# Optimization experiments

Hardware: AMD Instinct MI355X
Metric: run time of the kernel (lower is better)

The kernel has to match this reference:

```python
import jax, jax.numpy as jnp
import numpy as np

N_NODES = 100000
N_EDGES = 1600000
IN_DIM = 256
HID = 128
FUSE = 64


def setup_inputs() -> dict:
    key = jax.random.key(0)
    ks = jax.random.split(key, 10)
    x = jax.random.normal(ks[0], (N_NODES, IN_DIM), dtype=jnp.float32)
    edge_index = jax.random.randint(ks[1], (2, N_EDGES), 0, N_NODES, dtype=jnp.int64)
    h_node = jax.random.normal(ks[2], (N_NODES,), dtype=jnp.float32)
    s = 0.05
    W_homo = jax.random.normal(ks[3], (IN_DIM, HID), dtype=jnp.float32) * s
    b_homo = jnp.zeros((HID,), dtype=jnp.float32)
    W_het = jax.random.normal(ks[4], (IN_DIM, HID), dtype=jnp.float32) * s
    b_het = jnp.zeros((HID,), dtype=jnp.float32)
    W_fuse = jax.random.normal(ks[5], (HID, FUSE), dtype=jnp.float32) * s
    b_fuse = jnp.zeros((FUSE,), dtype=jnp.float32)
    W_cls = jax.random.normal(ks[6], (FUSE, 2), dtype=jnp.float32) * s
    b_cls = jnp.zeros((2,), dtype=jnp.float32)
    return {
        "x": x, "edge_index": edge_index, "h_node": h_node,
        "W_homo": W_homo, "b_homo": b_homo,
        "W_het": W_het, "b_het": b_het,
        "W_fuse": W_fuse, "b_fuse": b_fuse,
        "W_cls": W_cls, "b_cls": b_cls,
    }


def gcn_conv(x, edge_index, W, b):
    # PyG GCNConv: xw = x @ W, add self-loops, symmetric D^-1/2 (A+I) D^-1/2 aggregation, + bias
    n = x.shape[0]
    xw = x @ W  # [N, H] transform first (in_dim > hid keeps edge traffic small)
    loop = jnp.arange(n, dtype=edge_index.dtype)
    src = jnp.concatenate([edge_index[0], loop])
    dst = jnp.concatenate([edge_index[1], loop])
    deg = jax.ops.segment_sum(jnp.ones_like(dst, dtype=xw.dtype), dst, num_segments=n)
    dinv = jnp.where(deg > 0, jax.lax.rsqrt(deg), 0.0)
    norm = dinv[src] * dinv[dst]  # [E+N]
    msg = xw[src] * norm[:, None]  # gather + scale  [E+N, H]
    agg = jax.ops.segment_sum(msg, dst, num_segments=n)  # scatter-add
    return agg + b


def reference(x, edge_index, h_node,
              W_homo, b_homo, W_het, b_het,
              W_fuse, b_fuse, W_cls, b_cls):
    h_homo = jax.nn.relu(gcn_conv(x, edge_index, W_homo, b_homo))
    h_het = jax.nn.relu(gcn_conv(x, edge_index, W_het, b_het))
    h_fused = 0.5 * h_homo + 0.5 * h_het  # fixed alpha = 0.5 (no het gate)
    h = jax.nn.relu(h_fused @ W_fuse + b_fuse)
    logits = h @ W_cls + b_cls
    return logits
```

## Files before the change

kernel.cpp:

```cpp
#include <hip/hip_runtime.h>

#define IN_DIM 256
#define CHUNK 8192
#define NBUCKET 1024

typedef __attribute__((ext_vector_type(8))) short short8;
typedef __attribute__((ext_vector_type(4))) float f32x4;
typedef unsigned int uint;
typedef unsigned short ushort;

__device__ __forceinline__ ushort f2bf(float x) {
    uint u = __float_as_uint(x);
    u += 0x7FFFu + ((u >> 16) & 1u);
    return (ushort)(u >> 16);
}

__global__ __launch_bounds__(256) void hist_kernel(const int* __restrict__ dst,
                                                   int* __restrict__ hist_g,
                                                   int E, int NBLK) {
    __shared__ int h[NBUCKET];
    int tid = threadIdx.x;
#pragma unroll
    for (int i = 0; i < 4; ++i) h[tid + 256 * i] = 0;
    __syncthreads();
    int base = blockIdx.x * CHUNK;
#pragma unroll 4
    for (int i = 0; i < 32; ++i) {
        int e = base + i * 256 + tid;
        if (e < E) atomicAdd(&h[dst[e] >> 7], 1);
    }
    __syncthreads();
#pragma unroll
    for (int i = 0; i < 4; ++i) {
        int b = tid + 256 * i;
        hist_g[(size_t)b * NBLK + blockIdx.x] = h[b];
    }
}

__global__ __launch_bounds__(256) void block_sum_kernel(const int* __restrict__ d,
                                                        int* __restrict__ bsum, int L) {
    __shared__ int red[256];
    int base = blockIdx.x * 1024;
    int s = 0;
    for (int i = threadIdx.x; i < 1024; i += 256) {
        int idx = base + i;
        if (idx < L) s += d[idx];
    }
    red[threadIdx.x] = s;
    __syncthreads();
    for (int dd = 128; dd > 0; dd >>= 1) {
        if (threadIdx.x < dd) red[threadIdx.x] += red[threadIdx.x + dd];
        __syncthreads();
    }
    if (threadIdx.x == 0) bsum[blockIdx.x] = red[0];
}

__global__ __launch_bounds__(1024) void scan_sums_kernel(int* __restrict__ bsum, int B) {
    __shared__ int sh[1024];
    int t = threadIdx.x;
    sh[t] = (t < B) ? bsum[t] : 0;
    __syncthreads();
    for (int d = 1; d < 1024; d <<= 1) {
        int v = (t >= d) ? sh[t - d] : 0;
        __syncthreads();
        sh[t] += v;
        __syncthreads();
    }
    if (t < B) bsum[t] = (t == 0) ? 0 : sh[t - 1];
}

__global__ __launch_bounds__(256) void scan_apply_kernel(int* __restrict__ d,
                                                         const int* __restrict__ bsum, int L) {
    __shared__ int wsum[4];
    int lane = threadIdx.x & 63, wid = threadIdx.x >> 6;
    int idx = blockIdx.x * 1024 + threadIdx.x * 4;
    int c[4];
    int s = 0;
#pragma unroll
    for (int j = 0; j < 4; ++j) {
        c[j] = (idx + j < L) ? d[idx + j] : 0;
        s += c[j];
    }
    int incl = s;
#pragma unroll
    for (int dd = 1; dd < 64; dd <<= 1) {
        int v = __shfl_up(incl, dd);
        if (lane >= dd) incl += v;
    }
    if (lane == 63) wsum[wid] = incl;
    __syncthreads();
    int woff = 0;
    for (int i = 0; i < 4; ++i) woff += (i < wid) ? wsum[i] : 0;
    int excl = bsum[blockIdx.x] + woff + incl - s;
#pragma unroll
    for (int j = 0; j < 4; ++j) {
        if (idx + j < L) d[idx + j] = excl;
        excl += c[j];
    }
}

__global__ __launch_bounds__(256) void scatter_kernel(const int* __restrict__ ei,
                                                      const int* __restrict__ scanned,
                                                      uint2* __restrict__ sorted,
                                                      int E, int NBLK) {
    __shared__ int baseh[NBUCKET];
    __shared__ int curh[NBUCKET];
    int tid = threadIdx.x;
#pragma unroll
    for (int i = 0; i < 4; ++i) {
        int b = tid + 256 * i;
        baseh[b] = scanned[(size_t)b * NBLK + blockIdx.x];
        curh[b] = 0;
    }
    __syncthreads();
    int base = blockIdx.x * CHUNK;
#pragma unroll 4
    for (int i = 0; i < 32; ++i) {
        int e = base + i * 256 + tid;
        if (e < E) {
            int s = ei[e];
            int d = ei[E + e];
            int b = d >> 7;
            int r = atomicAdd(&curh[b], 1);
            sorted[baseh[b] + r] = make_uint2((uint)s, (uint)d);
        }
    }
}

__global__ __launch_bounds__(256) void bucket_csr_kernel(const uint2* __restrict__ sorted,
                                                         const int* __restrict__ scanned,
                                                         int* __restrict__ off,
                                                         int* __restrict__ csr,
                                                         float* __restrict__ dinv,
                                                         int N, int E, int NBLK) {
    __shared__ int cnt[128], cur[128];
    __shared__ int w0tot;
    int b = blockIdx.x;
    int tid = threadIdx.x;
    int estart = scanned[(size_t)b * NBLK];
    int eend = scanned[(size_t)(b + 1) * NBLK];
    if (tid < 128) cnt[tid] = 0;
    __syncthreads();
    for (int e = estart + tid; e < eend; e += 256)
        atomicAdd(&cnt[sorted[e].y & 127], 1);
    __syncthreads();
    int c = 0, incl = 0;
    if (tid < 128) {
        int lane = tid & 63;
        c = cnt[tid];
        incl = c;
#pragma unroll
        for (int d = 1; d < 64; d <<= 1) {
            int v = __shfl_up(incl, d);
            if (lane >= d) incl += v;
        }
        if (tid == 63) w0tot = incl;
    }
    __syncthreads();
    if (tid < 128) {
        int e0 = incl - c + ((tid >= 64) ? w0tot : 0);
        cur[tid] = e0;
        int node = b * 128 + tid;
        if (node < N) {
            off[node] = estart + e0;
            dinv[node] = rsqrtf((float)(c + 1));
        }
    }
    if (b == 0 && tid == 0) off[N] = E;
    __syncthreads();
    for (int e = estart + tid; e < eend; e += 256) {
        uint2 sd = sorted[e];
        int pos = atomicAdd(&cur[sd.y & 127], 1);
        csr[estart + pos] = (int)sd.x;
    }
}

__global__ void prep_kernel(const float* __restrict__ Wh, const float* __restrict__ Wt,
                            const float* __restrict__ Wf,
                            ushort* __restrict__ wT, ushort* __restrict__ WfB) {
    int b = blockIdx.x;
    int k = threadIdx.x;
    if (b < 256) {
        const float* W = (b < 128) ? Wh : Wt;
        wT[b * 256 + k] = f2bf(W[(size_t)k * 128 + (b & 127)]);
    } else {
        int col = b - 256;
        if (k < 128) WfB[col * 128 + k] = f2bf(Wf[(size_t)k * 64 + col]);
    }
}

__global__ __launch_bounds__(512) void gemm_kernel(const float* __restrict__ x,
                                                   const ushort* __restrict__ wT,
                                                   const float* __restrict__ dinv,
                                                   ushort* __restrict__ y, int N) {
    __shared__ short As[128 * 64];
    __shared__ short Bs[256 * 64];
    int tid = threadIdx.x;
    int lane = tid & 63, wid = tid >> 6;
    int wr = wid >> 2, wc = wid & 3;
    int rowBase = blockIdx.x * 128;

    f32x4 acc[4][4];
#pragma unroll
    for (int a = 0; a < 4; ++a)
#pragma unroll
        for (int b = 0; b < 4; ++b) acc[a][b] = (f32x4){0.f, 0.f, 0.f, 0.f};

    for (int k0 = 0; k0 < IN_DIM; k0 += 64) {
        __syncthreads();
#pragma unroll
        for (int r = 0; r < 2; ++r) {
            int id = tid + r * 512;
            int m = id >> 3, kc = id & 7;
            int gr = rowBase + m; if (gr >= N) gr = N - 1;
            const float* src = x + (size_t)gr * IN_DIM + k0 + kc * 8;
            float4 v0 = *(const float4*)src;
            float4 v1 = *(const float4*)(src + 4);
            short8 pk;
            pk[0] = (short)f2bf(v0.x); pk[1] = (short)f2bf(v0.y);
            pk[2] = (short)f2bf(v0.z); pk[3] = (short)f2bf(v0.w);
            pk[4] = (short)f2bf(v1.x); pk[5] = (short)f2bf(v1.y);
            pk[6] = (short)f2bf(v1.z); pk[7] = (short)f2bf(v1.w);
            *(short8*)&As[(m * 8 + (kc ^ (m & 7))) * 8] = pk;
        }
#pragma unroll
        for (int r = 0; r < 4; ++r) {
            int id = tid + r * 512;
            int n = id >> 3, kc = id & 7;
            short8 v = *(const short8*)(wT + n * 256 + k0 + kc * 8);
            *(short8*)&Bs[(n * 8 + (kc ^ (n & 7))) * 8] = v;
        }
        __syncthreads();

#pragma unroll
        for (int kk = 0; kk < 2; ++kk) {
            int cpos = kk * 4 + (lane >> 4);
            short8 af[4], bfr[4];
#pragma unroll
            for (int mf = 0; mf < 4; ++mf) {
                int m = wr * 64 + mf * 16 + (lane & 15);
                af[mf] = *(const short8*)&As[(m * 8 + (cpos ^ (m & 7))) * 8];
            }
#pragma unroll
            for (int nf = 0; nf < 4; ++nf) {
                int n = wc * 64 + nf * 16 + (lane & 15);
                bfr[nf] = *(const short8*)&Bs[(n * 8 + (cpos ^ (n & 7))) * 8];
            }
#pragma unroll
            for (int mf = 0; mf < 4; ++mf)
#pragma unroll
                for (int nf = 0; nf < 4; ++nf)
                    acc[mf][nf] = __builtin_amdgcn_mfma_f32_16x16x32_bf16(
                        af[mf], bfr[nf], acc[mf][nf], 0, 0, 0);
        }
    }

#pragma unroll
    for (int mf = 0; mf < 4; ++mf)
#pragma unroll
        for (int i = 0; i < 4; ++i) {
            int row = rowBase + wr * 64 + mf * 16 + ((lane >> 4) << 2) + i;
            if (row < N) {
                float dv = dinv[row];
#pragma unroll
                for (int nf = 0; nf < 4; ++nf)
                    y[(size_t)row * IN_DIM + wc * 64 + nf * 16 + (lane & 15)] =
                        f2bf(acc[mf][nf][i] * dv);
            }
        }
}

__global__ __launch_bounds__(256) void gather_kernel(const ushort* __restrict__ y,
                                                     const int* __restrict__ off,
                                                     const int* __restrict__ csr,
                                                     const float* __restrict__ bh,
                                                     const float* __restrict__ bt,
                                                     ushort* __restrict__ f, int N) {
    int tid = threadIdx.x;
    int lane = tid & 63, wid = tid >> 6;
    const float* bp = (lane < 32) ? (bh + lane * 4) : (bt + (lane - 32) * 4);
    float4 b4 = *(const float4*)bp;
    int n = blockIdx.x * 4 + wid;
    int stride = gridDim.x * 4;

    for (; n < N; n += stride) {
        int e0 = off[n], e1 = off[n + 1];
        int deg = e1 - e0;
        float a0, a1, a2, a3;
        {
            uint2 sv = *(const uint2*)(y + (size_t)n * 256 + lane * 4);
            a0 = __uint_as_float(sv.x << 16);
            a1 = __uint_as_float(sv.x & 0xffff0000u);
            a2 = __uint_as_float(sv.y << 16);
            a3 = __uint_as_float(sv.y & 0xffff0000u);
        }
        for (int base = 0; base < deg; base += 64) {
            int rem = deg - base;
            int iters = rem < 64 ? rem : 64;
            int sAll = csr[e0 + base + (lane < iters ? lane : iters - 1)];
            for (int i = 0; i < iters; i += 4) {
                int idx[4], s[4];
                float sc[4];
#pragma unroll
                for (int k = 0; k < 4; ++k) {
                    idx[k] = (i + k < iters) ? i + k : iters - 1;
                    sc[k] = (i + k < iters) ? 1.f : 0.f;
                }
#pragma unroll
                for (int k = 0; k < 4; ++k) s[k] = __builtin_amdgcn_readlane(sAll, idx[k]);
                uint2 v[4];
#pragma unroll
                for (int k = 0; k < 4; ++k)
                    v[k] = *(const uint2*)(y + (size_t)s[k] * 256 + lane * 4);
                a0 += __uint_as_float(v[0].x << 16);
                a1 += __uint_as_float(v[0].x & 0xffff0000u);
                a2 += __uint_as_float(v[0].y << 16);
                a3 += __uint_as_float(v[0].y & 0xffff0000u);
#pragma unroll
                for (int k = 1; k < 4; ++k) {
                    a0 = fmaf(__uint_as_float(v[k].x << 16), sc[k], a0);
                    a1 = fmaf(__uint_as_float(v[k].x & 0xffff0000u), sc[k], a1);
                    a2 = fmaf(__uint_as_float(v[k].y << 16), sc[k], a2);
                    a3 = fmaf(__uint_as_float(v[k].y & 0xffff0000u), sc[k], a3);
                }
            }
        }
        float dv = rsqrtf((float)(deg + 1));
        float r0 = fmaxf(fmaf(a0, dv, b4.x), 0.f);
        float r1 = fmaxf(fmaf(a1, dv, b4.y), 0.f);
        float r2 = fmaxf(fmaf(a2, dv, b4.z), 0.f);
        float r3 = fmaxf(fmaf(a3, dv, b4.w), 0.f);
        float o0 = __shfl_xor(r0, 32);
        float o1 = __shfl_xor(r1, 32);
        float o2 = __shfl_xor(r2, 32);
        float o3 = __shfl_xor(r3, 32);
        if (lane < 32) {
            float h0 = 0.5f * (r0 + o0);
            float h1 = 0.5f * (r1 + o1);
            float h2 = 0.5f * (r2 + o2);
            float h3 = 0.5f * (r3 + o3);
            uint2 pk;
            pk.x = (uint)f2bf(h0) | ((uint)f2bf(h1) << 16);
            pk.y = (uint)f2bf(h2) | ((uint)f2bf(h3) << 16);
            *(uint2*)(f + (size_t)n * 128 + lane * 4) = pk;
        }
    }
}

__global__ __launch_bounds__(256) void mlp_kernel(const ushort* __restrict__ f,
                                                  const ushort* __restrict__ WfB,
                                                  const float* __restrict__ bfu,
                                                  const float* __restrict__ Wc,
                                                  const float* __restrict__ bc,
                                                  float* __restrict__ out, int N) {
    int tid = threadIdx.x;
    int lane = tid & 63, wid = tid >> 6;
    int rowBase = blockIdx.x * 64 + wid * 16;
    int col = lane & 15;
    int kg = lane >> 4;

    short8 bfrag[4][4];
#pragma unroll
    for (int nf = 0; nf < 4; ++nf)
#pragma unroll
        for (int kk = 0; kk < 4; ++kk)
            bfrag[nf][kk] = *(const short8*)(WfB + (size_t)(nf * 16 + col) * 128 + kk * 32 + kg * 8);

    float bfv[4], w0[4], w1[4];
#pragma unroll
    for (int nf = 0; nf < 4; ++nf) {
        int c = nf * 16 + col;
        bfv[nf] = bfu[c];
        w0[nf] = Wc[c * 2];
        w1[nf] = Wc[c * 2 + 1];
    }
    float bc0 = bc[0], bc1 = bc[1];

    int r = rowBase + col; if (r >= N) r = N - 1;
    f32x4 acc[4];
#pragma unroll
    for (int nf = 0; nf < 4; ++nf) acc[nf] = (f32x4){0.f, 0.f, 0.f, 0.f};
#pragma unroll
    for (int kk = 0; kk < 4; ++kk) {
        short8 afrag = *(const short8*)(f + (size_t)r * 128 + kk * 32 + kg * 8);
#pragma unroll
        for (int nf = 0; nf < 4; ++nf)
            acc[nf] = __builtin_amdgcn_mfma_f32_16x16x32_bf16(afrag, bfrag[nf][kk], acc[nf], 0, 0, 0);
    }

#pragma unroll
    for (int i = 0; i < 4; ++i) {
        float p0 = 0.f, p1 = 0.f;
#pragma unroll
        for (int nf = 0; nf < 4; ++nf) {
            float t = fmaxf(acc[nf][i] + bfv[nf], 0.f);
            p0 = fmaf(t, w0[nf], p0);
            p1 = fmaf(t, w1[nf], p1);
        }
#pragma unroll
        for (int d = 1; d < 16; d <<= 1) {
            p0 += __shfl_xor(p0, d);
            p1 += __shfl_xor(p1, d);
        }
        int row = rowBase + kg * 4 + i;
        if (col == 0 && row < N)
            *(float2*)(out + (size_t)row * 2) = make_float2(p0 + bc0, p1 + bc1);
    }
}

extern "C" void kernel_launch(void* const* d_in, const int* in_sizes, int n_in,
                              void* d_out, int out_size, void* d_ws, size_t ws_size,
                              hipStream_t stream) {
    const float* x  = (const float*)d_in[0];
    const int*   ei = (const int*)d_in[1];
    const float* Wh = (const float*)d_in[3];
    const float* bh = (const float*)d_in[4];
    const float* Wt = (const float*)d_in[5];
    const float* bt = (const float*)d_in[6];
    const float* Wf = (const float*)d_in[7];
    const float* bf_ = (const float*)d_in[8];
    const float* Wc = (const float*)d_in[9];
    const float* bc = (const float*)d_in[10];
    float* out = (float*)d_out;

    int N = in_sizes[0] / IN_DIM;
    int E = in_sizes[1] / 2;
    int NBLK = (E + CHUNK - 1) / CHUNK;
    int L = NBUCKET * NBLK;
    int SB = (L + 1023) / 1024;
    int NBKT = (N + 127) / 128;

    char* w = (char*)d_ws;
    ushort* y    = (ushort*)w;  w += (size_t)N * IN_DIM * 2;
    ushort* wT   = (ushort*)w;  w += (size_t)256 * 256 * 2;
    ushort* WfB  = (ushort*)w;  w += (size_t)64 * 128 * 2;
    ushort* f    = (ushort*)w;  w += (size_t)N * 128 * 2;
    float* dinv  = (float*)w;   w += (size_t)N * 4;
    int*   off   = (int*)w;     w += (((size_t)(N + 1) * 4) + 15) & ~(size_t)15;
    int*   hist  = (int*)w;     w += (((size_t)L * 4) + 15) & ~(size_t)15;
    int*   bsum  = (int*)w;     w += (((size_t)SB * 4) + 15) & ~(size_t)15;
    uint2* sorted = (uint2*)w;  w += (size_t)E * 8;
    int*   csr   = (int*)w;     w += (size_t)E * 4;

    hist_kernel<<<NBLK, 256, 0, stream>>>(ei + E, hist, E, NBLK);
    block_sum_kernel<<<SB, 256, 0, stream>>>(hist, bsum, L);
    scan_sums_kernel<<<1, 1024, 0, stream>>>(bsum, SB);
    scan_apply_kernel<<<SB, 256, 0, stream>>>(hist, bsum, L);
    scatter_kernel<<<NBLK, 256, 0, stream>>>(ei, hist, sorted, E, NBLK);
    bucket_csr_kernel<<<NBKT, 256, 0, stream>>>(sorted, hist, off, csr, dinv, N, E, NBLK);
    prep_kernel<<<320, 256, 0, stream>>>(Wh, Wt, Wf, wT, WfB);

    gemm_kernel<<<(N + 127) / 128, 512, 0, stream>>>(x, wT, dinv, y, N);
    gather_kernel<<<2048, 256, 0, stream>>>(y, off, csr, bh, bt, f, N);
    mlp_kernel<<<(N + 63) / 64, 256, 0, stream>>>(f, WfB, bf_, Wc, bc, out, N);
}
```

Baseline: 229.6 us.

## Pack sorted edges into 32-bit words, use packed-float accumulation, double gather grid

The bucket-sorted edge buffer now stores one 32-bit word per edge, with the source in the low 20 bits and the local destination in the high bits, instead of an 8-byte pair. This halves that buffer's write and read traffic in the scatter and CSR kernels. The gather kernel accumulates in float2 vectors so the compiler can emit packed FP32 ops, and its grid is doubled. The bf16 conversion now uses the HIP intrinsic. The packing assumes node ids fit in 20 bits, which holds for 100000 nodes but not for graphs above about one million nodes.

```diff
diff --git a/kernel.cpp b/kernel.cpp
--- a/kernel.cpp
+++ b/kernel.cpp
@@ -1,4 +1,5 @@
 #include <hip/hip_runtime.h>
+#include <hip/hip_bf16.h>
 
 #define IN_DIM 256
 #define CHUNK 8192
@@ -6,13 +7,13 @@
 
 typedef __attribute__((ext_vector_type(8))) short short8;
 typedef __attribute__((ext_vector_type(4))) float f32x4;
+typedef __attribute__((ext_vector_type(2))) float f32x2;
 typedef unsigned int uint;
 typedef unsigned short ushort;
 
 __device__ __forceinline__ ushort f2bf(float x) {
-    uint u = __float_as_uint(x);
-    u += 0x7FFFu + ((u >> 16) & 1u);
-    return (ushort)(u >> 16);
+    __hip_bfloat16 h = __float2bfloat16(x);
+    return *reinterpret_cast<ushort*>(&h);
 }
 
 __global__ __launch_bounds__(256) void hist_kernel(const int* __restrict__ dst,
@@ -25,7 +26,7 @@
     __syncthreads();
     int base = blockIdx.x * CHUNK;
 #pragma unroll 4
-    for (int i = 0; i < 32; ++i) {
+    for (int i = 0; i < CHUNK / 256; ++i) {
         int e = base + i * 256 + tid;
         if (e < E) atomicAdd(&h[dst[e] >> 7], 1);
     }
@@ -101,7 +102,7 @@
 
 __global__ __launch_bounds__(256) void scatter_kernel(const int* __restrict__ ei,
                                                       const int* __restrict__ scanned,
-                                                      uint2* __restrict__ sorted,
+                                                      uint* __restrict__ sorted,
                                                       int E, int NBLK) {
     __shared__ int baseh[NBUCKET];
     __shared__ int curh[NBUCKET];
@@ -115,19 +116,19 @@
     __syncthreads();
     int base = blockIdx.x * CHUNK;
 #pragma unroll 4
-    for (int i = 0; i < 32; ++i) {
+    for (int i = 0; i < CHUNK / 256; ++i) {
         int e = base + i * 256 + tid;
         if (e < E) {
             int s = ei[e];
             int d = ei[E + e];
             int b = d >> 7;
             int r = atomicAdd(&curh[b], 1);
-            sorted[baseh[b] + r] = make_uint2((uint)s, (uint)d);
-        }
-    }
-}
-
-__global__ __launch_bounds__(256) void bucket_csr_kernel(const uint2* __restrict__ sorted,
+            sorted[baseh[b] + r] = (uint)s | ((uint)(d & 127) << 20);
+        }
+    }
+}
+
+__global__ __launch_bounds__(256) void bucket_csr_kernel(const uint* __restrict__ sorted,
                                                          const int* __restrict__ scanned,
                                                          int* __restrict__ off,
                                                          int* __restrict__ csr,
@@ -142,7 +143,7 @@
     if (tid < 128) cnt[tid] = 0;
     __syncthreads();
     for (int e = estart + tid; e < eend; e += 256)
-        atomicAdd(&cnt[sorted[e].y & 127], 1);
+        atomicAdd(&cnt[sorted[e] >> 20], 1);
     __syncthreads();
     int c = 0, incl = 0;
     if (tid < 128) {
@@ -169,9 +170,9 @@
     if (b == 0 && tid == 0) off[N] = E;
     __syncthreads();
     for (int e = estart + tid; e < eend; e += 256) {
-        uint2 sd = sorted[e];
-        int pos = atomicAdd(&cur[sd.y & 127], 1);
-        csr[estart + pos] = (int)sd.x;
+        uint pk = sorted[e];
+        int pos = atomicAdd(&cur[pk >> 20], 1);
+        csr[estart + pos] = (int)(pk & 0xFFFFFu);
     }
 }
 
@@ -286,13 +287,11 @@
     for (; n < N; n += stride) {
         int e0 = off[n], e1 = off[n + 1];
         int deg = e1 - e0;
-        float a0, a1, a2, a3;
+        f32x2 aA, aB;
         {
             uint2 sv = *(const uint2*)(y + (size_t)n * 256 + lane * 4);
-            a0 = __uint_as_float(sv.x << 16);
-            a1 = __uint_as_float(sv.x & 0xffff0000u);
-            a2 = __uint_as_float(sv.y << 16);
-            a3 = __uint_as_float(sv.y & 0xffff0000u);
+            aA = (f32x2){__uint_as_float(sv.x << 16), __uint_as_float(sv.x & 0xffff0000u)};
+            aB = (f32x2){__uint_as_float(sv.y << 16), __uint_as_float(sv.y & 0xffff0000u)};
         }
         for (int base = 0; base < deg; base += 64) {
             int rem = deg - base;
@@ -312,24 +311,22 @@
 #pragma unroll
                 for (int k = 0; k < 4; ++k)
                     v[k] = *(const uint2*)(y + (size_t)s[k] * 256 + lane * 4);
-                a0 += __uint_as_float(v[0].x << 16);
-                a1 += __uint_as_float(v[0].x & 0xffff0000u);
-                a2 += __uint_as_float(v[0].y << 16);
-                a3 += __uint_as_float(v[0].y & 0xffff0000u);
+                aA += (f32x2){__uint_as_float(v[0].x << 16), __uint_as_float(v[0].x & 0xffff0000u)};
+                aB += (f32x2){__uint_as_float(v[0].y << 16), __uint_as_float(v[0].y & 0xffff0000u)};
 #pragma unroll
                 for (int k = 1; k < 4; ++k) {
-                    a0 = fmaf(__uint_as_float(v[k].x << 16), sc[k], a0);
-                    a1 = fmaf(__uint_as_float(v[k].x & 0xffff0000u), sc[k], a1);
-                    a2 = fmaf(__uint_as_float(v[k].y << 16), sc[k], a2);
-                    a3 = fmaf(__uint_as_float(v[k].y & 0xffff0000u), sc[k], a3);
+                    f32x2 pA = {__uint_as_float(v[k].x << 16), __uint_as_float(v[k].x & 0xffff0000u)};
+                    f32x2 pB = {__uint_as_float(v[k].y << 16), __uint_as_float(v[k].y & 0xffff0000u)};
+                    aA += pA * sc[k];
+                    aB += pB * sc[k];
                 }
             }
         }
         float dv = rsqrtf((float)(deg + 1));
-        float r0 = fmaxf(fmaf(a0, dv, b4.x), 0.f);
-        float r1 = fmaxf(fmaf(a1, dv, b4.y), 0.f);
-        float r2 = fmaxf(fmaf(a2, dv, b4.z), 0.f);
-        float r3 = fmaxf(fmaf(a3, dv, b4.w), 0.f);
+        float r0 = fmaxf(fmaf(aA.x, dv, b4.x), 0.f);
+        float r1 = fmaxf(fmaf(aA.y, dv, b4.y), 0.f);
+        float r2 = fmaxf(fmaf(aB.x, dv, b4.z), 0.f);
+        float r3 = fmaxf(fmaf(aB.y, dv, b4.w), 0.f);
         float o0 = __shfl_xor(r0, 32);
         float o1 = __shfl_xor(r1, 32);
         float o2 = __shfl_xor(r2, 32);
@@ -439,7 +436,7 @@
     int*   off   = (int*)w;     w += (((size_t)(N + 1) * 4) + 15) & ~(size_t)15;
     int*   hist  = (int*)w;     w += (((size_t)L * 4) + 15) & ~(size_t)15;
     int*   bsum  = (int*)w;     w += (((size_t)SB * 4) + 15) & ~(size_t)15;
-    uint2* sorted = (uint2*)w;  w += (size_t)E * 8;
+    uint*  sorted = (uint*)w;   w += (size_t)E * 4;
     int*   csr   = (int*)w;     w += (size_t)E * 4;
 
     hist_kernel<<<NBLK, 256, 0, stream>>>(ei + E, hist, E, NBLK);
@@ -451,6 +448,6 @@
     prep_kernel<<<320, 256, 0, stream>>>(Wh, Wt, Wf, wT, WfB);
 
     gemm_kernel<<<(N + 127) / 128, 512, 0, stream>>>(x, wT, dinv, y, N);
-    gather_kernel<<<2048, 256, 0, stream>>>(y, off, csr, bh, bt, f, N);
+    gather_kernel<<<4096, 256, 0, stream>>>(y, off, csr, bh, bt, f, N);
     mlp_kernel<<<(N + 63) / 64, 256, 0, stream>>>(f, WfB, bf_, Wc, bc, out, N);
 }
```

After: 226.1 us. Within noise of the previous version (-1.5%).
